# Kernel optimization log

Measured on AMD Instinct MI355X. Metric: run time of the kernel, lower is better.

The kernel has to match this reference:

```python
import jax, jax.numpy as jnp
import numpy as np

NPERSEG = 512
STEP = 256
NSEG = 9            # frames for L=2048 with boundary='zeros', padded=True
NFREQ = 257
NUM_FILTER = 2
PI = 3.1415926      # same constant as source

_win = 0.5 * (1.0 - jnp.cos(2.0 * jnp.pi * jnp.arange(NPERSEG, dtype=jnp.float32) / NPERSEG))  # periodic hann (scipy get_window('hann'))
_win_sum = 256.0    # sum of periodic hann, exact


def _stft(x):
    # x: (B, D, L) real -> scipy.signal.stft(..., nperseg=512, noverlap=256) => (B, D, 257, 9)
    xp = jnp.pad(x, ((0, 0), (0, 0), (STEP, STEP)))  # boundary='zeros'
    idx = jnp.arange(NSEG)[:, None] * STEP + jnp.arange(NPERSEG)[None, :]
    frames = xp[..., idx] * _win                     # (B,D,9,512)
    Z = jnp.fft.rfft(frames, axis=-1) / _win_sum     # scaling='spectrum'
    return jnp.swapaxes(Z, -1, -2)                   # (B,D,257,9)


def _istft(Z):
    # Z: (B,D,257,9) complex -> (B,D,2048) real (scipy.signal.istft inverse)
    xs = jnp.fft.irfft(jnp.swapaxes(Z, -1, -2) * _win_sum, n=NPERSEG, axis=-1) * _win  # (B,D,9,512)
    total = NPERSEG + (NSEG - 1) * STEP  # 2560
    idx = (jnp.arange(NSEG)[:, None] * STEP + jnp.arange(NPERSEG)[None, :]).reshape(-1)
    B, D = Z.shape[0], Z.shape[1]
    x = jnp.zeros((B, D, total), xs.dtype).at[..., idx].add(xs.reshape(B, D, -1))
    norm = jnp.zeros((total,), jnp.float32).at[idx].add(jnp.tile(_win ** 2, NSEG))
    x = x / jnp.where(norm > 1e-10, norm, 1.0)
    return x[..., STEP:total - STEP]  # trim boundary padding -> length 2048


def _cplx(p):
    return p[..., 0] + 1j * p[..., 1]  # torch.view_as_complex


def _filter(x, length, bank):
    # x: (B,S,D) complex; bank: (K,S,D,2). power = x*x/length (complex square, as in source)
    power = x * x / length
    k = jnp.arange(NUM_FILTER, dtype=jnp.float32)
    coef = jnp.cos((2.0 * (k + 1.0) - 1.0) * PI / 2.0 * NUM_FILTER)  # matches source precedence
    return jnp.sum(power[None] * _cplx(bank)[:, None] * coef[:, None, None, None], axis=0)


def _ln(x, g, b):
    m = jnp.mean(x, -1, keepdims=True)
    v = jnp.mean((x - m) ** 2, -1, keepdims=True)
    return (x - m) * jax.lax.rsqrt(v + 1e-5) * g + b


def _addnorm(x, g1, b1, w1, bb1, w2, bb2, g2, b2):
    x = _ln(x, g1, b1)
    h = jax.nn.gelu(x @ w1.T + bb1, approximate=False)  # torch GELU (exact)
    return _ln(h @ w2.T + bb2 + x, g2, b2)


def setup_inputs() -> dict:
    key = jax.random.key(0)
    ks = jax.random.split(key, 12)
    B, D = 8, 768
    d = {}
    d['ecg'] = jax.random.normal(ks[0], (B, 2048, D), jnp.float32)
    d['image'] = jax.random.normal(ks[1], (B, 196, D), jnp.float32)
    d['ecg_filter_bank'] = jax.random.normal(ks[2], (2, 2313, D, 2), jnp.float32)
    d['cxr_filter_bank'] = jax.random.normal(ks[3], (2, 99, D, 2), jnp.float32)
    d['gate_sel'] = jax.random.normal(ks[4], (99, D, 2), jnp.float32)
    d['gate_w'] = jax.random.normal(ks[5], (D, D), jnp.float32) * 0.02
    d['gate_b'] = jnp.zeros((D,), jnp.float32)
    for i, p in enumerate(['e', 'c']):
        d[p + '_ln1_g'] = jnp.ones((D,), jnp.float32)
        d[p + '_ln1_b'] = jnp.zeros((D,), jnp.float32)
        d[p + '_w1'] = jax.random.normal(ks[6 + 2 * i], (D, D), jnp.float32) * 0.02
        d[p + '_b1'] = jnp.zeros((D,), jnp.float32)
        d[p + '_w2'] = jax.random.normal(ks[7 + 2 * i], (D, D), jnp.float32) * 0.02
        d[p + '_b2'] = jnp.zeros((D,), jnp.float32)
        d[p + '_ln2_g'] = jnp.ones((D,), jnp.float32)
        d[p + '_ln2_b'] = jnp.zeros((D,), jnp.float32)
    return d


def reference(ecg, image, ecg_filter_bank, cxr_filter_bank, gate_sel, gate_w, gate_b,
              e_ln1_g, e_ln1_b, e_w1, e_b1, e_w2, e_b2, e_ln2_g, e_ln2_b,
              c_ln1_g, c_ln1_b, c_w1, c_b1, c_w2, c_b2, c_ln2_g, c_ln2_b):
    B, S, D = ecg.shape
    N = image.shape[1]
    # STFT path (source detaches to CPU -> stop_gradient)
    Z = _stft(jnp.swapaxes(jax.lax.stop_gradient(ecg), 1, 2))       # (B,D,257,9)
    _ecg = jnp.transpose(Z, (0, 2, 3, 1)).reshape(B, NFREQ * NSEG, D)
    _img = jnp.fft.rfft(image, axis=1, norm='ortho')                # (B,99,D)
    _ecg = _filter(_ecg, NFREQ * NSEG, ecg_filter_bank)
    _img = _filter(_img, N // 2 + 1, cxr_filter_bank)
    # Cxr2EcgGate: complex selection, avgpool over spatial (real part), 1x1 conv
    gate = jnp.mean((_img * _cplx(gate_sel)).real, axis=1) @ gate_w.T + gate_b  # (B,D)
    ecg_g = _ecg * gate[:, None, :]
    # NOTE: source overwrites gated image with irfft of filtered _image (ecg_gate output unused)
    img_t = jnp.fft.irfft(_img, n=N, axis=1, norm='ortho')          # (B,N,D)
    Zg = jnp.transpose(ecg_g.reshape(B, NFREQ, NSEG, D), (0, 3, 1, 2))
    ecg_t = jnp.swapaxes(_istft(jax.lax.stop_gradient(Zg)), 1, 2)   # (B,2048,D); source detaches before istft
    text = _addnorm(ecg_t + ecg, e_ln1_g, e_ln1_b, e_w1, e_b1, e_w2, e_b2, e_ln2_g, e_ln2_b)
    img = _addnorm(img_t + image, c_ln1_g, c_ln1_b, c_w1, c_b1, c_w2, c_b2, c_ln2_g, c_ln2_b)
    return (text, img)
```

## Files before the change

kernel.cpp:

```cpp
#include <hip/hip_runtime.h>
#include <math.h>

namespace {

constexpr int B_ = 8;
constexpr int S_ = 2048;
constexpr int D_ = 768;
constexpr int N_ = 196;
constexpr int NF_ = 99;
constexpr int NFREQ_ = 257;
constexpr int NSEG_ = 9;
constexpr int NBINS_ = NFREQ_ * NSEG_;
constexpr int NW_ = D_ * D_;
constexpr float TWOPI_ = 6.28318530717958647692f;

using bf16x8 = __attribute__((ext_vector_type(8))) short;
using f32x4  = __attribute__((ext_vector_type(4))) float;

__device__ __forceinline__ int rev9(int x) { return (int)(__brev((unsigned)x) >> 23); }
__device__ __forceinline__ int padz(int i) { return i + (i >> 4); }

__device__ __forceinline__ unsigned short f2bf(float x) {
  unsigned u = __float_as_uint(x);
  u = (u + 0x7FFFu + ((u >> 16) & 1u)) >> 16;
  return (unsigned short)u;
}
__device__ __forceinline__ float bf2f(unsigned short h) {
  return __uint_as_float(((unsigned)h) << 16);
}

__device__ __forceinline__ float gelu_f(float v) {
  const float x = fabsf(v) * 0.70710678118654752440f;
  const float t = 1.0f / fmaf(0.3275911f, x, 1.0f);
  float p = fmaf(fmaf(fmaf(fmaf(1.061405429f, t, -1.453152027f), t, 1.421413741f),
                      t, -0.284496736f), t, 0.254829592f);
  const float e = __expf(-x * x);
  const float er = 1.0f - p * t * e;
  return 0.5f * v * (1.0f + ((v < 0.f) ? -er : er));
}

__device__ __forceinline__ void gload16(const void* g, void* l) {
  __builtin_amdgcn_global_load_lds((const __attribute__((address_space(1))) void*)g,
                                   (__attribute__((address_space(3))) void*)l, 16, 0, 0);
}

__device__ __forceinline__ float2 cmulf(float2 a, float2 b) {
  return make_float2(a.x * b.x - a.y * b.y, a.x * b.y + a.y * b.x);
}
__device__ __forceinline__ float2 cadd(float2 a, float2 b) {
  return make_float2(a.x + b.x, a.y + b.y);
}
__device__ __forceinline__ float2 csub(float2 a, float2 b) {
  return make_float2(a.x - b.x, a.y - b.y);
}

__global__ __launch_bounds__(256) void k_transpose_g(const float* __restrict__ src,
                                                     float* __restrict__ dst,
                                                     int R, int C) {
  __shared__ float tile[32][33];
  const int b = blockIdx.z;
  const int c0 = blockIdx.x * 32;
  const int r0 = blockIdx.y * 32;
  const int tx = threadIdx.x & 31, ty = threadIdx.x >> 5;
  for (int i = ty; i < 32; i += 8)
    tile[i][tx] = src[((size_t)b * R + r0 + i) * C + c0 + tx];
  __syncthreads();
  for (int i = ty; i < 32; i += 8)
    dst[((size_t)b * C + c0 + i) * R + r0 + tx] = tile[tx][i];
}

constexpr int PREP_W = (NW_ + 255) / 256;
constexpr int PREP_WALL = 4 * PREP_W;
constexpr int PREP_FC = (NBINS_ * D_ + 255) / 256;
__global__ __launch_bounds__(256) void k_prep(
    const float* __restrict__ w0, const float* __restrict__ w1,
    const float* __restrict__ w2, const float* __restrict__ w3,
    unsigned short* __restrict__ wbf, const float2* __restrict__ e2,
    float2* __restrict__ FcT, float2* __restrict__ twg) {
  const int bid = blockIdx.x;
  if (bid < PREP_WALL) {
    const int m = bid / PREP_W;
    const int i = (bid - m * PREP_W) * 256 + threadIdx.x;
    if (i >= NW_) return;
    const float* src = (m == 0) ? w0 : (m == 1) ? w1 : (m == 2) ? w2 : w3;
    wbf[(size_t)m * NW_ + i] = f2bf(src[i]);
  } else if (bid < PREP_WALL + PREP_FC) {
    const int o = (bid - PREP_WALL) * 256 + threadIdx.x;
    if (o >= NBINS_ * D_) return;
    const int d = o / NBINS_;
    const int r = o - d * NBINS_;
    const int f = r / NFREQ_;
    const int k = r - f * NFREQ_;
    const int s = k * 9 + f;
    const float2 a = e2[(size_t)s * D_ + d];
    const float2 b = e2[(size_t)(NBINS_ + s) * D_ + d];
    FcT[o] = make_float2(-(a.x + b.x), -(a.y + b.y));
  } else {
    const int i = (bid - PREP_WALL - PREP_FC) * 256 + threadIdx.x;
    if (i >= 511) return;
    const int v = i + 1;
    const int h = 1 << (31 - __clz(v));
    const int j = v - h;
    float sn, cs;
    sincosf((float)j * ((TWOPI_ * 0.5f) / (float)h), &sn, &cs);
    twg[i] = make_float2(cs, sn);
  }
}

__global__ __launch_bounds__(256) void k_img_dft_f(
    const float* __restrict__ image, const float2* __restrict__ bank2,
    const float2* __restrict__ gsel2, float2* __restrict__ imgF,
    float* __restrict__ part) {
  const int fg = blockIdx.x;
  const int f0 = fg * 9;
  const int d = blockIdx.y * 256 + threadIdx.x;
  const int b = blockIdx.z;
  __shared__ float2 tws[9 * N_];
  for (int idx = threadIdx.x; idx < 9 * N_; idx += 256) {
    const int fi = idx / N_;
    const int t = idx - fi * N_;
    const int r = ((f0 + fi) * t) % N_;
    float sn, cs;
    sincosf(TWOPI_ * (float)r / (float)N_, &sn, &cs);
    tws[idx] = make_float2(cs, sn);
  }
  __syncthreads();
  float re[9] = {}, im[9] = {};
  const float* ip = image + (size_t)b * N_ * D_ + d;
  for (int t = 0; t < N_; ++t) {
    const float v = ip[(size_t)t * D_];
#pragma unroll
    for (int fi = 0; fi < 9; ++fi) {
      const float2 w = tws[fi * N_ + t];
      re[fi] = fmaf(v, w.x, re[fi]);
      im[fi] = fmaf(-v, w.y, im[fi]);
    }
  }
  const float sc = 1.0f / (196.0f * 99.0f);
  float gp = 0.f;
#pragma unroll
  for (int fi = 0; fi < 9; ++fi) {
    const int f = f0 + fi;
    const float pr = (re[fi] * re[fi] - im[fi] * im[fi]) * sc;
    const float pi2 = (2.f * re[fi] * im[fi]) * sc;
    const size_t fd = (size_t)f * D_ + d;
    const float2 c0 = bank2[fd];
    const float2 c1 = bank2[(size_t)NF_ * D_ + fd];
    const float fcr = -(c0.x + c1.x), fci = -(c0.y + c1.y);
    const float zr = pr * fcr - pi2 * fci;
    const float zi = pr * fci + pi2 * fcr;
    imgF[(size_t)(b * NF_ + f) * D_ + d] = make_float2(zr, zi);
    const float2 gw = gsel2[fd];
    gp += zr * gw.x - zi * gw.y;
  }
  part[((size_t)b * 11 + fg) * D_ + d] = gp;
}

__global__ __launch_bounds__(256) void k_gate_mm2(const float* __restrict__ part,
                                                  const float* __restrict__ W,
                                                  const float* __restrict__ bias,
                                                  float* __restrict__ gate) {
  __shared__ float row[8][D_];
  __shared__ float red[16][16][8];
  const int tid = threadIdx.x;
  const int d0 = blockIdx.x * 16;
  for (int i = tid; i < 8 * D_; i += 256) {
    const int b = i / D_, e = i - b * D_;
    float s = 0.f;
    for (int p = 0; p < 11; ++p) s += part[((size_t)b * 11 + p) * D_ + e];
    row[b][e] = s * (1.0f / 99.0f);
  }
  __syncthreads();
  const int dl = tid >> 4;
  const int ec = tid & 15;
  const float* w = W + (size_t)(d0 + dl) * D_ + ec * 48;
  float acc[8] = {};
  for (int e = 0; e < 48; e += 4) {
    const float4 wv = *reinterpret_cast<const float4*>(w + e);
    const int eg = ec * 48 + e;
#pragma unroll
    for (int b = 0; b < 8; ++b) {
      acc[b] = fmaf(row[b][eg], wv.x, acc[b]);
      acc[b] = fmaf(row[b][eg + 1], wv.y, acc[b]);
      acc[b] = fmaf(row[b][eg + 2], wv.z, acc[b]);
      acc[b] = fmaf(row[b][eg + 3], wv.w, acc[b]);
    }
  }
#pragma unroll
  for (int b = 0; b < 8; ++b) red[dl][ec][b] = acc[b];
  __syncthreads();
  if (tid < 128) {
    const int dl2 = tid >> 3, b = tid & 7;
    float s = bias[d0 + dl2];
    for (int c = 0; c < 16; ++c) s += red[dl2][c][b];
    gate[b * D_ + d0 + dl2] = s;
  }
}

__global__ __launch_bounds__(256) void k_img_idft(
    const float2* __restrict__ imgF, const float* __restrict__ image,
    float* __restrict__ xi) {
  const int t0 = blockIdx.x * 14;
  const int d = blockIdx.y * 256 + threadIdx.x;
  const int b = blockIdx.z;
  __shared__ float2 tws[14 * NF_];
  for (int idx = threadIdx.x; idx < 14 * NF_; idx += 256) {
    const int ti = idx / NF_;
    const int f = idx - ti * NF_;
    const int r = ((t0 + ti) * f) % N_;
    float sn, cs;
    sincosf(TWOPI_ * (float)r / (float)N_, &sn, &cs);
    tws[idx] = make_float2(cs, sn);
  }
  __syncthreads();
  const float2* zp = imgF + (size_t)b * NF_ * D_ + d;
  const float2 z0 = zp[0];
  const float2 zny = zp[(size_t)(NF_ - 1) * D_];
  float acc[14];
#pragma unroll
  for (int ti = 0; ti < 14; ++ti)
    acc[ti] = z0.x + (((t0 + ti) & 1) ? -zny.x : zny.x);
  for (int f = 1; f < NF_ - 1; ++f) {
    const float2 z = zp[(size_t)f * D_];
#pragma unroll
    for (int ti = 0; ti < 14; ++ti) {
      const float2 w = tws[ti * NF_ + f];
      acc[ti] += 2.f * (z.x * w.x - z.y * w.y);
    }
  }
#pragma unroll
  for (int ti = 0; ti < 14; ++ti) {
    const size_t idx = (size_t)(b * N_ + t0 + ti) * D_ + d;
    xi[idx] = acc[ti] * (1.0f / 14.0f) + image[idx];
  }
}

__global__ __launch_bounds__(256) void k_layernorm_f2b(const float* __restrict__ x,
                                                       const float* __restrict__ g,
                                                       const float* __restrict__ b,
                                                       unsigned short* __restrict__ out) {
  const int row = blockIdx.x;
  const int tid = threadIdx.x;
  const float* xr = x + (size_t)row * D_;
  const float v0 = xr[tid], v1 = xr[tid + 256], v2 = xr[tid + 512];
  float s = v0 + v1 + v2;
  float q = v0 * v0 + v1 * v1 + v2 * v2;
  __shared__ float red[8];
  for (int off = 32; off > 0; off >>= 1) {
    s += __shfl_down(s, off);
    q += __shfl_down(q, off);
  }
  if ((tid & 63) == 0) { red[tid >> 6] = s; red[4 + (tid >> 6)] = q; }
  __syncthreads();
  s = red[0] + red[1] + red[2] + red[3];
  q = red[4] + red[5] + red[6] + red[7];
  const float mean = s * (1.0f / 768.0f);
  const float var = q * (1.0f / 768.0f) - mean * mean;
  const float inv = rsqrtf(var + 1e-5f);
  unsigned short* orow = out + (size_t)row * D_;
  orow[tid]       = f2bf((v0 - mean) * inv * g[tid]       + b[tid]);
  orow[tid + 256] = f2bf((v1 - mean) * inv * g[tid + 256] + b[tid + 256]);
  orow[tid + 512] = f2bf((v2 - mean) * inv * g[tid + 512] + b[tid + 512]);
}

template <int H, int DIR, bool TRIV>
__device__ __forceinline__ void pass8(float2* z, int l,
                                      float2 wa, float2 wb, float2 wc) {
  asm volatile("s_waitcnt lgkmcnt(0)" ::: "memory");
  const float sg = (DIR < 0) ? -1.f : 1.f;
  const int base = (H == 1) ? (l << 3)
                 : (H == 8) ? (((l >> 3) << 6) | (l & 7))
                            : l;
  const float2 x0 = z[padz(base)],         x1 = z[padz(base + H)];
  const float2 x2 = z[padz(base + 2 * H)], x3 = z[padz(base + 3 * H)];
  const float2 x4 = z[padz(base + 4 * H)], x5 = z[padz(base + 5 * H)];
  const float2 x6 = z[padz(base + 6 * H)], x7 = z[padz(base + 7 * H)];
  const float2 WA = make_float2(wa.x, sg * wa.y);
  const float2 WB = make_float2(wb.x, sg * wb.y);
  const float2 WC = make_float2(wc.x, sg * wc.y);
  const float2 WBp = make_float2(-sg * WB.y, sg * WB.x);
  float2 t, u;
  t = TRIV ? x1 : cmulf(x1, WA); const float2 A0 = cadd(x0, t), A1 = csub(x0, t);
  t = TRIV ? x3 : cmulf(x3, WA); const float2 A2 = cadd(x2, t), A3 = csub(x2, t);
  t = TRIV ? x5 : cmulf(x5, WA); const float2 A4 = cadd(x4, t), A5 = csub(x4, t);
  t = TRIV ? x7 : cmulf(x7, WA); const float2 A6 = cadd(x6, t), A7 = csub(x6, t);
  t = TRIV ? A2 : cmulf(A2, WB);
  u = TRIV ? make_float2(-sg * A3.y, sg * A3.x) : cmulf(A3, WBp);
  const float2 B0 = cadd(A0, t), B2 = csub(A0, t);
  const float2 B1 = cadd(A1, u), B3 = csub(A1, u);
  t = TRIV ? A6 : cmulf(A6, WB);
  u = TRIV ? make_float2(-sg * A7.y, sg * A7.x) : cmulf(A7, WBp);
  const float2 B4 = cadd(A4, t), B6 = csub(A4, t);
  const float2 B5 = cadd(A5, u), B7 = csub(A5, u);
  const float r_ = 0.70710678118654752440f;
  const float2 F1 = TRIV ? make_float2(r_, sg * r_)
                         : cmulf(WC, make_float2(r_, sg * r_));
  const float2 F2 = TRIV ? make_float2(0.f, sg)
                         : make_float2(-sg * WC.y, sg * WC.x);
  const float2 F3 = TRIV ? make_float2(-r_, sg * r_)
                         : cmulf(WC, make_float2(-r_, sg * r_));
  t = TRIV ? B4 : cmulf(B4, WC);
  z[padz(base)]         = cadd(B0, t);
  z[padz(base + 4 * H)] = csub(B0, t);
  t = cmulf(B5, F1);
  z[padz(base + H)]     = cadd(B1, t);
  z[padz(base + 5 * H)] = csub(B1, t);
  t = cmulf(B6, F2);
  z[padz(base + 2 * H)] = cadd(B2, t);
  z[padz(base + 6 * H)] = csub(B2, t);
  t = cmulf(B7, F3);
  z[padz(base + 3 * H)] = cadd(B3, t);
  z[padz(base + 7 * H)] = csub(B3, t);
}

template <int FA, int FB>
__device__ __forceinline__ void scatter_buf(float2* z, const float (&s)[8],
                                            float wlo, float whi, int rlo, int rhi) {
  constexpr int iAlo = (FA > 0) ? FA - 1 : 0;
  constexpr int iAhi = (FA < 8) ? FA : 0;
  constexpr int iBlo = (FB > 0) ? FB - 1 : 0;
  constexpr int iBhi = (FB >= 0 && FB < 8) ? FB : 0;
  const float aLo = (FA == 0) ? 0.f : s[iAlo] * wlo;
  const float aHi = (FA == 8) ? 0.f : s[iAhi] * whi;
  const float bLo = (FB <= 0) ? 0.f : s[iBlo] * wlo;
  const float bHi = (FB < 0 || FB == 8) ? 0.f : s[iBhi] * whi;
  z[rlo] = make_float2(aLo, bLo);
  z[rhi] = make_float2(aHi, bHi);
}

template <int FA, int FB>
__device__ __forceinline__ void filt_pack(const float2* z, int k, float g,
                                          float2 cA, float2 cB,
                                          float2& Ck, float2& Cm) {
  const int q = (512 - k) & 511;
  const float2 Zk = z[padz(k)], Zq = z[padz(q)];
  const float sc = 0.5f / 256.f;
  const float ar = (Zk.x + Zq.x) * sc, ai = (Zk.y - Zq.y) * sc;
  float yar, yai, ybr = 0.f, ybi = 0.f;
  {
    const float pr = (ar * ar - ai * ai) * (1.f / 2313.f);
    const float pi = (2.f * ar * ai) * (1.f / 2313.f);
    yar = (pr * cA.x - pi * cA.y) * g;
    yai = (pr * cA.y + pi * cA.x) * g;
  }
  if (FB >= 0) {
    const float br = (Zk.y + Zq.y) * sc, bi = (Zq.x - Zk.x) * sc;
    const float pr = (br * br - bi * bi) * (1.f / 2313.f);
    const float pi = (2.f * br * bi) * (1.f / 2313.f);
    ybr = (pr * cB.x - pi * cB.y) * g;
    ybi = (pr * cB.y + pi * cB.x) * g;
  }
  if (k == 0 || k == 256) {
    Ck = make_float2(yar, ybr);
    Cm = Ck;
  } else {
    Ck = make_float2(yar - ybi, yai + ybr);
    Cm = make_float2(yar + ybi, ybr - yai);
  }
}

template <int FA0, int FB0, int FA1, int FB1, int FA2, int FB2, int FA3, int FB3,
          int NBUF>
__device__ __forceinline__ void ecg_super4(int tid, float g,
                                           const float2* __restrict__ fc,
                                           const float (&s)[8], const float2 (&ptw)[6],
                                           float2 t8, float2* zA, float2* zB,
                                           float2* zC, float2* zD, float* accr) {
  const float c0 = t8.x;
  const float wlo = 0.5f - 0.5f * c0;
  const float whi = 0.5f + 0.5f * c0;
  float2 cA0 = fc[FA0 * 257 + tid];
  float2 cB0 = make_float2(0.f, 0.f), cA1 = cB0, cB1 = cB0;
  float2 cA2 = cB0, cB2 = cB0, cA3 = cB0, cB3 = cB0;
  if (FB0 >= 0) cB0 = fc[FB0 * 257 + tid];
  if (NBUF > 1) { cA1 = fc[FA1 * 257 + tid]; cB1 = fc[FB1 * 257 + tid]; }
  if (NBUF > 2) { cA2 = fc[FA2 * 257 + tid]; cB2 = fc[FB2 * 257 + tid]; }
  if (NBUF > 3) { cA3 = fc[FA3 * 257 + tid]; cB3 = fc[FB3 * 257 + tid]; }
  __syncthreads();
  const int rlo = padz(rev9(tid)), rhi = padz(rev9(tid + 256));
  scatter_buf<FA0, FB0>(zA, s, wlo, whi, rlo, rhi);
  if (NBUF > 1) scatter_buf<FA1, FB1>(zB, s, wlo, whi, rlo, rhi);
  if (NBUF > 2) scatter_buf<FA2, FB2>(zC, s, wlo, whi, rlo, rhi);
  if (NBUF > 3) scatter_buf<FA3, FB3>(zD, s, wlo, whi, rlo, rhi);
  __syncthreads();
  const int wid = tid >> 6, l = tid & 63;
  if (wid < NBUF) {
    float2* zz = (wid == 0) ? zA : (wid == 1) ? zB : (wid == 2) ? zC : zD;
    pass8<1, -1, true>(zz, l, ptw[0], ptw[1], ptw[2]);
    pass8<8, -1, false>(zz, l, ptw[0], ptw[1], ptw[2]);
    pass8<64, -1, false>(zz, l, ptw[3], ptw[4], ptw[5]);
  }
  __syncthreads();
  float2 Ck0, Cm0, Ck1, Cm1, Ck2, Cm2, Ck3, Cm3;
  float2 Cn0, Cn1, Cn2, Cn3, dum;
  filt_pack<FA0, FB0>(zA, tid, g, cA0, cB0, Ck0, Cm0);
  if (NBUF > 1) filt_pack<FA1, FB1>(zB, tid, g, cA1, cB1, Ck1, Cm1);
  if (NBUF > 2) filt_pack<FA2, FB2>(zC, tid, g, cA2, cB2, Ck2, Cm2);
  if (NBUF > 3) filt_pack<FA3, FB3>(zD, tid, g, cA3, cB3, Ck3, Cm3);
  if (tid == 0) {
    float2 nA, nB = make_float2(0.f, 0.f);
    nA = fc[FA0 * 257 + 256];
    if (FB0 >= 0) nB = fc[FB0 * 257 + 256];
    filt_pack<FA0, FB0>(zA, 256, g, nA, nB, Cn0, dum);
    if (NBUF > 1) {
      nA = fc[FA1 * 257 + 256]; nB = fc[FB1 * 257 + 256];
      filt_pack<FA1, FB1>(zB, 256, g, nA, nB, Cn1, dum);
    }
    if (NBUF > 2) {
      nA = fc[FA2 * 257 + 256]; nB = fc[FB2 * 257 + 256];
      filt_pack<FA2, FB2>(zC, 256, g, nA, nB, Cn2, dum);
    }
    if (NBUF > 3) {
      nA = fc[FA3 * 257 + 256]; nB = fc[FB3 * 257 + 256];
      filt_pack<FA3, FB3>(zD, 256, g, nA, nB, Cn3, dum);
    }
  }
  __syncthreads();
  {
    zA[rlo] = Ck0;
    if (NBUF > 1) zB[rlo] = Ck1;
    if (NBUF > 2) zC[rlo] = Ck2;
    if (NBUF > 3) zD[rlo] = Ck3;
    if (tid == 0) {
      zA[padz(1)] = Cn0;
      if (NBUF > 1) zB[padz(1)] = Cn1;
      if (NBUF > 2) zC[padz(1)] = Cn2;
      if (NBUF > 3) zD[padz(1)] = Cn3;
    } else {
      const int rm = padz(rev9(512 - tid));
      zA[rm] = Cm0;
      if (NBUF > 1) zB[rm] = Cm1;
      if (NBUF > 2) zC[rm] = Cm2;
      if (NBUF > 3) zD[rm] = Cm3;
    }
  }
  __syncthreads();
  if (wid < NBUF) {
    float2* zz = (wid == 0) ? zA : (wid == 1) ? zB : (wid == 2) ? zC : zD;
    pass8<1, 1, true>(zz, l, ptw[0], ptw[1], ptw[2]);
    pass8<8, 1, false>(zz, l, ptw[0], ptw[1], ptw[2]);
    pass8<64, 1, false>(zz, l, ptw[3], ptw[4], ptw[5]);
  }
  __syncthreads();
  {
    const float2 vLo = zA[padz(tid)], vHi = zA[padz(tid + 256)];
    accr[FA0] += 0.5f * wlo * vLo.x;
    accr[FA0 + 1] += 0.5f * whi * vHi.x;
    if (FB0 >= 0) {
      accr[FB0] += 0.5f * wlo * vLo.y;
      accr[FB0 + 1] += 0.5f * whi * vHi.y;
    }
    if (NBUF > 1) {
      const float2 uLo = zB[padz(tid)], uHi = zB[padz(tid + 256)];
      accr[FA1] += 0.5f * wlo * uLo.x;
      accr[FA1 + 1] += 0.5f * whi * uHi.x;
      accr[FB1] += 0.5f * wlo * uLo.y;
      accr[FB1 + 1] += 0.5f * whi * uHi.y;
    }
    if (NBUF > 2) {
      const float2 uLo = zC[padz(tid)], uHi = zC[padz(tid + 256)];
      accr[FA2] += 0.5f * wlo * uLo.x;
      accr[FA2 + 1] += 0.5f * whi * uHi.x;
      accr[FB2] += 0.5f * wlo * uLo.y;
      accr[FB2 + 1] += 0.5f * whi * uHi.y;
    }
    if (NBUF > 3) {
      const float2 uLo = zD[padz(tid)], uHi = zD[padz(tid + 256)];
      accr[FA3] += 0.5f * wlo * uLo.x;
      accr[FA3 + 1] += 0.5f * whi * uHi.x;
      accr[FB3] += 0.5f * wlo * uLo.y;
      accr[FB3 + 1] += 0.5f * whi * uHi.y;
    }
  }
}

__global__ __launch_bounds__(256) void k_ecg_fft(
    const float* __restrict__ ecgT, const float2* __restrict__ FcT,
    const float* __restrict__ gate, const float2* __restrict__ twg,
    unsigned short* __restrict__ xtT) {
  const int bd = blockIdx.x;
  const int d = bd % D_;
  const int tid = threadIdx.x;

  __shared__ float2 zA[544], zB[544], zC[544], zD[544];

  float s[8];
  const float* src = ecgT + (size_t)bd * S_;
#pragma unroll
  for (int k = 0; k < 8; ++k) s[k] = src[k * 256 + tid];

  const int l6 = tid & 63;
  float2 ptw[6];
  ptw[0] = twg[7 + (l6 & 7)];
  ptw[1] = twg[15 + (l6 & 7)];
  ptw[2] = twg[31 + (l6 & 7)];
  ptw[3] = twg[63 + l6];
  ptw[4] = twg[127 + l6];
  ptw[5] = twg[255 + l6];
  const float2 t8 = twg[255 + tid];

  const float g = gate[bd];
  const float2* fc = FcT + (size_t)d * NBINS_;
  float accr[10];
#pragma unroll
  for (int i = 0; i < 10; ++i) accr[i] = 0.f;

  ecg_super4<0, 8, 1, 2, 3, 4, 5, 6, 4>(tid, g, fc, s, ptw, t8, zA, zB, zC, zD, accr);
  ecg_super4<7, -1, 0, 0, 0, 0, 0, 0, 1>(tid, g, fc, s, ptw, t8, zA, zB, zC, zD, accr);

  const float c0 = t8.x;
  const float rinv = 1.0f / (0.5f + 0.5f * c0 * c0);
  unsigned short* dst = xtT + (size_t)bd * S_;
#pragma unroll
  for (int i2 = 0; i2 < 8; ++i2)
    dst[i2 * 256 + tid] = f2bf(accr[i2 + 1] * rinv + s[i2]);
}

__global__ __launch_bounds__(256) void k_colstats_bf(const unsigned short* __restrict__ xtT,
                                                     float2* __restrict__ stats) {
  const int b = blockIdx.y;
  const int t0 = blockIdx.x * 128;
  const int tx = threadIdx.x & 63;
  const int ty = threadIdx.x >> 6;
  float s0 = 0.f, q0 = 0.f, s1 = 0.f, q1 = 0.f;
  const unsigned int* base = (const unsigned int*)(xtT + (size_t)b * D_ * S_);
  for (int dd = ty; dd < D_; dd += 4) {
    const unsigned int u = base[(size_t)dd * (S_ / 2) + (t0 >> 1) + tx];
    const float v0 = bf2f((unsigned short)(u & 0xffffu));
    const float v1 = bf2f((unsigned short)(u >> 16));
    s0 += v0; q0 = fmaf(v0, v0, q0);
    s1 += v1; q1 = fmaf(v1, v1, q1);
  }
  __shared__ float sh[4][64][4];
  sh[ty][tx][0] = s0; sh[ty][tx][1] = q0; sh[ty][tx][2] = s1; sh[ty][tx][3] = q1;
  __syncthreads();
  if (ty == 0) {
    s0 = sh[0][tx][0] + sh[1][tx][0] + sh[2][tx][0] + sh[3][tx][0];
    q0 = sh[0][tx][1] + sh[1][tx][1] + sh[2][tx][1] + sh[3][tx][1];
    s1 = sh[0][tx][2] + sh[1][tx][2] + sh[2][tx][2] + sh[3][tx][2];
    q1 = sh[0][tx][3] + sh[1][tx][3] + sh[2][tx][3] + sh[3][tx][3];
    stats[(size_t)b * S_ + t0 + 2 * tx]     = make_float2(s0, q0);
    stats[(size_t)b * S_ + t0 + 2 * tx + 1] = make_float2(s1, q1);
  }
}

__global__ __launch_bounds__(256) void k_transpose_ln(
    const unsigned short* __restrict__ xtT, const float2* __restrict__ stats,
    const float* __restrict__ g, const float* __restrict__ bia,
    unsigned short* __restrict__ xhat) {
  __shared__ float tile[32][33];
  const int b = blockIdx.z;
  const int t0 = blockIdx.x * 32;
  const int d0 = blockIdx.y * 32;
  const int tx = threadIdx.x & 31, ty = threadIdx.x >> 5;
  for (int i = ty; i < 32; i += 8)
    tile[i][tx] = bf2f(xtT[((size_t)b * D_ + d0 + i) * S_ + t0 + tx]);
  __syncthreads();
  const float gv = g[d0 + tx], bv = bia[d0 + tx];
  for (int i = ty; i < 32; i += 8) {
    const float2 st = stats[(size_t)b * S_ + t0 + i];
    const float mean = st.x * (1.0f / 768.0f);
    const float var = st.y * (1.0f / 768.0f) - mean * mean;
    const float inv = rsqrtf(var + 1e-5f);
    xhat[((size_t)b * S_ + t0 + i) * D_ + d0 + tx] =
        f2bf((tile[tx][i] - mean) * inv * gv + bv);
  }
}

__global__ __launch_bounds__(256) void k_layernorm_dual(
    const unsigned short* __restrict__ x1, const float* __restrict__ g1,
    const float* __restrict__ b1, float* __restrict__ o1, int n1,
    const unsigned short* __restrict__ x2, const float* __restrict__ g2,
    const float* __restrict__ b2, float* __restrict__ o2) {
  int row = blockIdx.x;
  const unsigned short* x; const float *g, *b; float* o;
  if (row < n1) { x = x1; g = g1; b = b1; o = o1; }
  else { row -= n1; x = x2; g = g2; b = b2; o = o2; }
  const int tid = threadIdx.x;
  const unsigned short* xr = x + (size_t)row * D_;
  const float v0 = bf2f(xr[tid]), v1 = bf2f(xr[tid + 256]), v2 = bf2f(xr[tid + 512]);
  float s = v0 + v1 + v2;
  float q = v0 * v0 + v1 * v1 + v2 * v2;
  __shared__ float red[8];
  for (int off = 32; off > 0; off >>= 1) {
    s += __shfl_down(s, off);
    q += __shfl_down(q, off);
  }
  if ((tid & 63) == 0) { red[tid >> 6] = s; red[4 + (tid >> 6)] = q; }
  __syncthreads();
  s = red[0] + red[1] + red[2] + red[3];
  q = red[4] + red[5] + red[6] + red[7];
  const float mean = s * (1.0f / 768.0f);
  const float var = q * (1.0f / 768.0f) - mean * mean;
  const float inv = rsqrtf(var + 1e-5f);
  float* orow = o + (size_t)row * D_;
  orow[tid]       = (v0 - mean) * inv * g[tid]       + b[tid];
  orow[tid + 256] = (v1 - mean) * inv * g[tid + 256] + b[tid + 256];
  orow[tid + 512] = (v2 - mean) * inv * g[tid + 512] + b[tid + 512];
}

template <int MODE>
__global__ __launch_bounds__(256) void k_gemm_dual(
    const unsigned short* __restrict__ A1, const unsigned short* __restrict__ W1,
    const float* __restrict__ b1, const unsigned short* __restrict__ r1,
    unsigned short* __restrict__ o1, int M1, int nby1,
    const unsigned short* __restrict__ A2, const unsigned short* __restrict__ W2,
    const float* __restrict__ b2, const unsigned short* __restrict__ r2,
    unsigned short* __restrict__ o2, int M2) {
  __shared__ unsigned short Asm[2][128 * 64];
  __shared__ unsigned short Bsm[2][128 * 64];
  const int tid = threadIdx.x;
  const int lane = tid & 63, wid = tid >> 6;
  const int wr = wid >> 1, wc = wid & 1;
  int bx, by;
  {
    const int nwg = gridDim.x * gridDim.y;
    const int bid = blockIdx.y * gridDim.x + blockIdx.x;
    const int xcd = bid & 7, lin = bid >> 3;
    const int qq = nwg >> 3, rr = nwg & 7;
    const int nbid = (xcd < rr) ? xcd * (qq + 1) + lin
                                : rr * (qq + 1) + (xcd - rr) * qq + lin;
    bx = nbid % gridDim.x;
    by = nbid / gridDim.x;
  }
  const unsigned short* Abf; const unsigned short* Wbf; const float* bias;
  const unsigned short* resid; unsigned short* outb; int M;
  if (by < nby1) { Abf = A1; Wbf = W1; bias = b1; resid = r1; outb = o1; M = M1; }
  else { by -= nby1; Abf = A2; Wbf = W2; bias = b2; resid = r2; outb = o2; M = M2; }
  const int n0 = bx * 128, m0 = by * 128;

  auto STAGE = [&](int buf, int kt) {
    const int k0 = kt * 64;
#pragma unroll
    for (int i = 0; i < 4; ++i) {
      const int c = tid + 256 * i;
      const int row = c >> 3, sl = c & 7;
      const int gsl = sl ^ (row & 7);
      gload16(Abf + (size_t)(m0 + row) * 768 + k0 + gsl * 8, &Asm[buf][c * 8]);
      gload16(Wbf + (size_t)(n0 + row) * 768 + k0 + gsl * 8, &Bsm[buf][c * 8]);
    }
  };

  f32x4 acc[4][4] = {};
  STAGE(0, 0);
  for (int kt = 0; kt < 12; ++kt) {
    const int cur = kt & 1;
    if (kt < 11) {
      STAGE(cur ^ 1, kt + 1);
      asm volatile("s_waitcnt vmcnt(8)" ::: "memory");
    } else {
      asm volatile("s_waitcnt vmcnt(0)" ::: "memory");
    }
    __builtin_amdgcn_sched_barrier(0);
    __builtin_amdgcn_s_barrier();
#pragma unroll
    for (int ks = 0; ks < 2; ++ks) {
      bf16x8 af[4], bfv[4];
#pragma unroll
      for (int mi = 0; mi < 4; ++mi) {
        const int row = wr * 64 + mi * 16 + (lane & 15);
        const int sl = (ks * 4 + (lane >> 4)) ^ (row & 7);
        af[mi] = *(const bf16x8*)((const char*)Asm[cur] + row * 128 + sl * 16);
      }
#pragma unroll
      for (int ni = 0; ni < 4; ++ni) {
        const int row = wc * 64 + ni * 16 + (lane & 15);
        const int sl = (ks * 4 + (lane >> 4)) ^ (row & 7);
        bfv[ni] = *(const bf16x8*)((const char*)Bsm[cur] + row * 128 + sl * 16);
      }
#pragma unroll
      for (int mi = 0; mi < 4; ++mi)
#pragma unroll
        for (int ni = 0; ni < 4; ++ni)
          acc[mi][ni] = __builtin_amdgcn_mfma_f32_16x16x32_bf16(af[mi], bfv[ni],
                                                                acc[mi][ni], 0, 0, 0);
    }
    __builtin_amdgcn_sched_barrier(0);
    __builtin_amdgcn_s_barrier();
  }
#pragma unroll
  for (int mi = 0; mi < 4; ++mi) {
#pragma unroll
    for (int ni = 0; ni < 4; ++ni) {
      const int col = n0 + wc * 64 + ni * 16 + (lane & 15);
#pragma unroll
      for (int e = 0; e < 4; ++e) {
        const int row = m0 + wr * 64 + mi * 16 + (lane >> 4) * 4 + e;
        if (row >= M) continue;
        float v = acc[mi][ni][e] + bias[col];
        if (MODE == 0) {
          v = gelu_f(v);
        } else {
          v += bf2f(resid[(size_t)row * 768 + col]);
        }
        outb[(size_t)row * 768 + col] = f2bf(v);
      }
    }
  }
}

}

extern "C" void kernel_launch(void* const* d_in, const int* in_sizes, int n_in,
                              void* d_out, int out_size, void* d_ws, size_t ws_size,
                              hipStream_t stream) {
  (void)in_sizes; (void)n_in; (void)out_size; (void)ws_size;
  const float* ecg     = (const float*)d_in[0];
  const float* image   = (const float*)d_in[1];
  const float* ebank   = (const float*)d_in[2];
  const float* cbank   = (const float*)d_in[3];
  const float* gsel    = (const float*)d_in[4];
  const float* gw      = (const float*)d_in[5];
  const float* gb      = (const float*)d_in[6];
  const float* e_ln1_g = (const float*)d_in[7];
  const float* e_ln1_b = (const float*)d_in[8];
  const float* e_w1    = (const float*)d_in[9];
  const float* e_b1    = (const float*)d_in[10];
  const float* e_w2    = (const float*)d_in[11];
  const float* e_b2    = (const float*)d_in[12];
  const float* e_ln2_g = (const float*)d_in[13];
  const float* e_ln2_b = (const float*)d_in[14];
  const float* c_ln1_g = (const float*)d_in[15];
  const float* c_ln1_b = (const float*)d_in[16];
  const float* c_w1    = (const float*)d_in[17];
  const float* c_b1    = (const float*)d_in[18];
  const float* c_w2    = (const float*)d_in[19];
  const float* c_b2    = (const float*)d_in[20];
  const float* c_ln2_g = (const float*)d_in[21];
  const float* c_ln2_b = (const float*)d_in[22];

  float* out = (float*)d_out;
  float* ws = (float*)d_ws;

  constexpr size_t TXT = (size_t)8 * 2048 * 768;
  constexpr size_t IMG = (size_t)8 * 196 * 768;

  float* A  = ws;
  float* Bb = A + TXT;
  unsigned short* wbf = (unsigned short*)(Bb + TXT);
  unsigned short* ew1b = wbf;
  unsigned short* ew2b = wbf + NW_;
  unsigned short* cw1b = wbf + 2 * NW_;
  unsigned short* cw2b = wbf + 3 * NW_;
  float* gatev = (float*)(wbf + 4 * (size_t)NW_);
  float2* stats = (float2*)(gatev + 8 * 768);
  float* gpart = (float*)(stats + 8 * 2048);
  float2* twg = (float2*)(gpart + 8 * 11 * 768);

  float2* FcT = (float2*)out;

  unsigned short* xhat = (unsigned short*)A;
  unsigned short* y_tb = (unsigned short*)A + TXT;
  unsigned short* xtT = (unsigned short*)Bb;
  unsigned short* h_t = (unsigned short*)Bb;
  float* Bb2 = Bb + TXT / 2;
  float2* imgF = (float2*)Bb2;
  float* xi = Bb2 + 1216512;
  unsigned short* xh_i = (unsigned short*)(xi + IMG);
  unsigned short* h_i  = xh_i + IMG;
  unsigned short* y_ib = h_i + IMG;

  k_prep<<<PREP_WALL + PREP_FC + 2, 256, 0, stream>>>(
      e_w1, e_w2, c_w1, c_w2, wbf, (const float2*)ebank, FcT, twg);

  k_img_dft_f<<<dim3(11, 3, 8), 256, 0, stream>>>(image, (const float2*)cbank,
                                                  (const float2*)gsel, imgF, gpart);
  k_gate_mm2<<<48, 256, 0, stream>>>(gpart, gw, gb, gatev);
  k_img_idft<<<dim3(14, 3, 8), 256, 0, stream>>>(imgF, image, xi);
  k_layernorm_f2b<<<1568, 256, 0, stream>>>(xi, c_ln1_g, c_ln1_b, xh_i);

  k_transpose_g<<<dim3(24, 64, 8), 256, 0, stream>>>(ecg, A, 2048, 768);
  k_ecg_fft<<<8 * 768, 256, 0, stream>>>(A, FcT, gatev, twg, xtT);
  k_colstats_bf<<<dim3(16, 8), 256, 0, stream>>>(xtT, stats);
  k_transpose_ln<<<dim3(64, 24, 8), 256, 0, stream>>>(xtT, stats, e_ln1_g, e_ln1_b, xhat);

  k_gemm_dual<0><<<dim3(6, 141), 256, 0, stream>>>(
      xhat, ew1b, e_b1, nullptr, h_t, 16384, 128,
      xh_i, cw1b, c_b1, nullptr, h_i, 1568);
  k_gemm_dual<1><<<dim3(6, 141), 256, 0, stream>>>(
      h_t, ew2b, e_b2, xhat, y_tb, 16384, 128,
      h_i, cw2b, c_b2, xh_i, y_ib, 1568);
  k_layernorm_dual<<<16384 + 1568, 256, 0, stream>>>(
      y_tb, e_ln2_g, e_ln2_b, out, 16384,
      y_ib, c_ln2_g, c_ln2_b, out + TXT);
}
```

Before: 413.5 us.

## Pair two channels per block in ECG FFT to pack the odd ninth frame

The ECG STFT/filter/ISTFT kernel now handles two channels (d and d+384) per 512-thread block instead of one channel per 256-thread block. The first eight frames are packed two real frames per complex FFT across eight wavefronts. The leftover ninth frame from both channels is packed into one shared complex FFT, with a separate gate per half via a new gA/gB argument to filt_pack. This removes the round where only one wavefront was busy and halves the block count, at the cost of larger shared memory per block and extra barriers.

```diff
diff --git a/kernel.cpp b/kernel.cpp
--- a/kernel.cpp
+++ b/kernel.cpp
@@ -329,7 +329,7 @@
 }
 
 template <int FA, int FB>
-__device__ __forceinline__ void filt_pack(const float2* z, int k, float g,
+__device__ __forceinline__ void filt_pack(const float2* z, int k, float gA, float gB,
                                           float2 cA, float2 cB,
                                           float2& Ck, float2& Cm) {
   const int q = (512 - k) & 511;
@@ -340,15 +340,15 @@
   {
     const float pr = (ar * ar - ai * ai) * (1.f / 2313.f);
     const float pi = (2.f * ar * ai) * (1.f / 2313.f);
-    yar = (pr * cA.x - pi * cA.y) * g;
-    yai = (pr * cA.y + pi * cA.x) * g;
+    yar = (pr * cA.x - pi * cA.y) * gA;
+    yai = (pr * cA.y + pi * cA.x) * gA;
   }
   if (FB >= 0) {
     const float br = (Zk.y + Zq.y) * sc, bi = (Zq.x - Zk.x) * sc;
     const float pr = (br * br - bi * bi) * (1.f / 2313.f);
     const float pi = (2.f * br * bi) * (1.f / 2313.f);
-    ybr = (pr * cB.x - pi * cB.y) * g;
-    ybi = (pr * cB.y + pi * cB.x) * g;
+    ybr = (pr * cB.x - pi * cB.y) * gB;
+    ybi = (pr * cB.y + pi * cB.x) * gB;
   }
   if (k == 0 || k == 256) {
     Ck = make_float2(yar, ybr);
@@ -359,161 +359,171 @@
   }
 }
 
-template <int FA0, int FB0, int FA1, int FB1, int FA2, int FB2, int FA3, int FB3,
-          int NBUF>
-__device__ __forceinline__ void ecg_super4(int tid, float g,
-                                           const float2* __restrict__ fc,
-                                           const float (&s)[8], const float2 (&ptw)[6],
-                                           float2 t8, float2* zA, float2* zB,
-                                           float2* zC, float2* zD, float* accr) {
-  const float c0 = t8.x;
-  const float wlo = 0.5f - 0.5f * c0;
-  const float whi = 0.5f + 0.5f * c0;
-  float2 cA0 = fc[FA0 * 257 + tid];
-  float2 cB0 = make_float2(0.f, 0.f), cA1 = cB0, cB1 = cB0;
-  float2 cA2 = cB0, cB2 = cB0, cA3 = cB0, cB3 = cB0;
-  if (FB0 >= 0) cB0 = fc[FB0 * 257 + tid];
-  if (NBUF > 1) { cA1 = fc[FA1 * 257 + tid]; cB1 = fc[FB1 * 257 + tid]; }
-  if (NBUF > 2) { cA2 = fc[FA2 * 257 + tid]; cB2 = fc[FB2 * 257 + tid]; }
-  if (NBUF > 3) { cA3 = fc[FA3 * 257 + tid]; cB3 = fc[FB3 * 257 + tid]; }
-  __syncthreads();
-  const int rlo = padz(rev9(tid)), rhi = padz(rev9(tid + 256));
-  scatter_buf<FA0, FB0>(zA, s, wlo, whi, rlo, rhi);
-  if (NBUF > 1) scatter_buf<FA1, FB1>(zB, s, wlo, whi, rlo, rhi);
-  if (NBUF > 2) scatter_buf<FA2, FB2>(zC, s, wlo, whi, rlo, rhi);
-  if (NBUF > 3) scatter_buf<FA3, FB3>(zD, s, wlo, whi, rlo, rhi);
-  __syncthreads();
-  const int wid = tid >> 6, l = tid & 63;
-  if (wid < NBUF) {
-    float2* zz = (wid == 0) ? zA : (wid == 1) ? zB : (wid == 2) ? zC : zD;
-    pass8<1, -1, true>(zz, l, ptw[0], ptw[1], ptw[2]);
-    pass8<8, -1, false>(zz, l, ptw[0], ptw[1], ptw[2]);
-    pass8<64, -1, false>(zz, l, ptw[3], ptw[4], ptw[5]);
-  }
-  __syncthreads();
-  float2 Ck0, Cm0, Ck1, Cm1, Ck2, Cm2, Ck3, Cm3;
-  float2 Cn0, Cn1, Cn2, Cn3, dum;
-  filt_pack<FA0, FB0>(zA, tid, g, cA0, cB0, Ck0, Cm0);
-  if (NBUF > 1) filt_pack<FA1, FB1>(zB, tid, g, cA1, cB1, Ck1, Cm1);
-  if (NBUF > 2) filt_pack<FA2, FB2>(zC, tid, g, cA2, cB2, Ck2, Cm2);
-  if (NBUF > 3) filt_pack<FA3, FB3>(zD, tid, g, cA3, cB3, Ck3, Cm3);
-  if (tid == 0) {
-    float2 nA, nB = make_float2(0.f, 0.f);
-    nA = fc[FA0 * 257 + 256];
-    if (FB0 >= 0) nB = fc[FB0 * 257 + 256];
-    filt_pack<FA0, FB0>(zA, 256, g, nA, nB, Cn0, dum);
-    if (NBUF > 1) {
-      nA = fc[FA1 * 257 + 256]; nB = fc[FB1 * 257 + 256];
-      filt_pack<FA1, FB1>(zB, 256, g, nA, nB, Cn1, dum);
-    }
-    if (NBUF > 2) {
-      nA = fc[FA2 * 257 + 256]; nB = fc[FB2 * 257 + 256];
-      filt_pack<FA2, FB2>(zC, 256, g, nA, nB, Cn2, dum);
-    }
-    if (NBUF > 3) {
-      nA = fc[FA3 * 257 + 256]; nB = fc[FB3 * 257 + 256];
-      filt_pack<FA3, FB3>(zD, 256, g, nA, nB, Cn3, dum);
-    }
-  }
-  __syncthreads();
-  {
-    zA[rlo] = Ck0;
-    if (NBUF > 1) zB[rlo] = Ck1;
-    if (NBUF > 2) zC[rlo] = Ck2;
-    if (NBUF > 3) zD[rlo] = Ck3;
-    if (tid == 0) {
-      zA[padz(1)] = Cn0;
-      if (NBUF > 1) zB[padz(1)] = Cn1;
-      if (NBUF > 2) zC[padz(1)] = Cn2;
-      if (NBUF > 3) zD[padz(1)] = Cn3;
-    } else {
-      const int rm = padz(rev9(512 - tid));
-      zA[rm] = Cm0;
-      if (NBUF > 1) zB[rm] = Cm1;
-      if (NBUF > 2) zC[rm] = Cm2;
-      if (NBUF > 3) zD[rm] = Cm3;
-    }
-  }
-  __syncthreads();
-  if (wid < NBUF) {
-    float2* zz = (wid == 0) ? zA : (wid == 1) ? zB : (wid == 2) ? zC : zD;
-    pass8<1, 1, true>(zz, l, ptw[0], ptw[1], ptw[2]);
-    pass8<8, 1, false>(zz, l, ptw[0], ptw[1], ptw[2]);
-    pass8<64, 1, false>(zz, l, ptw[3], ptw[4], ptw[5]);
-  }
-  __syncthreads();
-  {
-    const float2 vLo = zA[padz(tid)], vHi = zA[padz(tid + 256)];
-    accr[FA0] += 0.5f * wlo * vLo.x;
-    accr[FA0 + 1] += 0.5f * whi * vHi.x;
-    if (FB0 >= 0) {
-      accr[FB0] += 0.5f * wlo * vLo.y;
-      accr[FB0 + 1] += 0.5f * whi * vHi.y;
-    }
-    if (NBUF > 1) {
-      const float2 uLo = zB[padz(tid)], uHi = zB[padz(tid + 256)];
-      accr[FA1] += 0.5f * wlo * uLo.x;
-      accr[FA1 + 1] += 0.5f * whi * uHi.x;
-      accr[FB1] += 0.5f * wlo * uLo.y;
-      accr[FB1 + 1] += 0.5f * whi * uHi.y;
-    }
-    if (NBUF > 2) {
-      const float2 uLo = zC[padz(tid)], uHi = zC[padz(tid + 256)];
-      accr[FA2] += 0.5f * wlo * uLo.x;
-      accr[FA2 + 1] += 0.5f * whi * uHi.x;
-      accr[FB2] += 0.5f * wlo * uLo.y;
-      accr[FB2 + 1] += 0.5f * whi * uHi.y;
-    }
-    if (NBUF > 3) {
-      const float2 uLo = zD[padz(tid)], uHi = zD[padz(tid + 256)];
-      accr[FA3] += 0.5f * wlo * uLo.x;
-      accr[FA3 + 1] += 0.5f * whi * uHi.x;
-      accr[FB3] += 0.5f * wlo * uLo.y;
-      accr[FB3 + 1] += 0.5f * whi * uHi.y;
-    }
-  }
-}
-
-__global__ __launch_bounds__(256) void k_ecg_fft(
+__global__ __launch_bounds__(512) void k_ecg_fft(
     const float* __restrict__ ecgT, const float2* __restrict__ FcT,
     const float* __restrict__ gate, const float2* __restrict__ twg,
     unsigned short* __restrict__ xtT) {
   const int bd = blockIdx.x;
-  const int d = bd % D_;
+  const int b = bd / 384, d0 = bd - (bd / 384) * 384;
   const int tid = threadIdx.x;
-
-  __shared__ float2 zA[544], zB[544], zC[544], zD[544];
+  const int grp = tid >> 8;
+  const int lt = tid & 255;
+  const int wid = tid >> 6;
+  const int l = tid & 63;
+  const int d = d0 + grp * 384;
+  const int myBD = b * 768 + d;
+
+  __shared__ float2 z[8][544];
 
   float s[8];
-  const float* src = ecgT + (size_t)bd * S_;
-#pragma unroll
-  for (int k = 0; k < 8; ++k) s[k] = src[k * 256 + tid];
-
-  const int l6 = tid & 63;
+  const float* src = ecgT + (size_t)myBD * S_;
+#pragma unroll
+  for (int k = 0; k < 8; ++k) s[k] = src[k * 256 + lt];
+
   float2 ptw[6];
-  ptw[0] = twg[7 + (l6 & 7)];
-  ptw[1] = twg[15 + (l6 & 7)];
-  ptw[2] = twg[31 + (l6 & 7)];
-  ptw[3] = twg[63 + l6];
-  ptw[4] = twg[127 + l6];
-  ptw[5] = twg[255 + l6];
-  const float2 t8 = twg[255 + tid];
-
-  const float g = gate[bd];
+  ptw[0] = twg[7 + (l & 7)];
+  ptw[1] = twg[15 + (l & 7)];
+  ptw[2] = twg[31 + (l & 7)];
+  ptw[3] = twg[63 + l];
+  ptw[4] = twg[127 + l];
+  ptw[5] = twg[255 + l];
+  const float2 t8 = twg[255 + lt];
+  const float c0 = t8.x;
+  const float wlo = 0.5f - 0.5f * c0;
+  const float whi = 0.5f + 0.5f * c0;
+  const int rlo = padz(rev9(lt)), rhi = padz(rev9(lt + 256));
+
+  const float gX = gate[b * 768 + d0];
+  const float gY = gate[b * 768 + d0 + 384];
+  const float gOwn = grp ? gY : gX;
   const float2* fc = FcT + (size_t)d * NBINS_;
+
   float accr[10];
 #pragma unroll
   for (int i = 0; i < 10; ++i) accr[i] = 0.f;
 
-  ecg_super4<0, 8, 1, 2, 3, 4, 5, 6, 4>(tid, g, fc, s, ptw, t8, zA, zB, zC, zD, accr);
-  ecg_super4<7, -1, 0, 0, 0, 0, 0, 0, 1>(tid, g, fc, s, ptw, t8, zA, zB, zC, zD, accr);
-
-  const float c0 = t8.x;
+  const float2 cA0 = fc[0 * 257 + lt], cB0 = fc[8 * 257 + lt];
+  const float2 cA1 = fc[1 * 257 + lt], cB1 = fc[2 * 257 + lt];
+  const float2 cA2 = fc[3 * 257 + lt], cB2 = fc[4 * 257 + lt];
+  const float2 cA3 = fc[5 * 257 + lt], cB3 = fc[6 * 257 + lt];
+  float2* zg = z[grp * 4];
+  scatter_buf<0, 8>(z[grp * 4 + 0], s, wlo, whi, rlo, rhi);
+  scatter_buf<1, 2>(z[grp * 4 + 1], s, wlo, whi, rlo, rhi);
+  scatter_buf<3, 4>(z[grp * 4 + 2], s, wlo, whi, rlo, rhi);
+  scatter_buf<5, 6>(z[grp * 4 + 3], s, wlo, whi, rlo, rhi);
+  __syncthreads();
+  {
+    float2* zz = z[wid];
+    pass8<1, -1, true>(zz, l, ptw[0], ptw[1], ptw[2]);
+    pass8<8, -1, false>(zz, l, ptw[0], ptw[1], ptw[2]);
+    pass8<64, -1, false>(zz, l, ptw[3], ptw[4], ptw[5]);
+  }
+  __syncthreads();
+  float2 Ck0, Cm0, Ck1, Cm1, Ck2, Cm2, Ck3, Cm3;
+  float2 Cn0, Cn1, Cn2, Cn3, dum;
+  filt_pack<0, 8>(z[grp * 4 + 0], lt, gOwn, gOwn, cA0, cB0, Ck0, Cm0);
+  filt_pack<1, 2>(z[grp * 4 + 1], lt, gOwn, gOwn, cA1, cB1, Ck1, Cm1);
+  filt_pack<3, 4>(z[grp * 4 + 2], lt, gOwn, gOwn, cA2, cB2, Ck2, Cm2);
+  filt_pack<5, 6>(z[grp * 4 + 3], lt, gOwn, gOwn, cA3, cB3, Ck3, Cm3);
+  if (lt == 0) {
+    float2 nA, nB;
+    nA = fc[0 * 257 + 256]; nB = fc[8 * 257 + 256];
+    filt_pack<0, 8>(z[grp * 4 + 0], 256, gOwn, gOwn, nA, nB, Cn0, dum);
+    nA = fc[1 * 257 + 256]; nB = fc[2 * 257 + 256];
+    filt_pack<1, 2>(z[grp * 4 + 1], 256, gOwn, gOwn, nA, nB, Cn1, dum);
+    nA = fc[3 * 257 + 256]; nB = fc[4 * 257 + 256];
+    filt_pack<3, 4>(z[grp * 4 + 2], 256, gOwn, gOwn, nA, nB, Cn2, dum);
+    nA = fc[5 * 257 + 256]; nB = fc[6 * 257 + 256];
+    filt_pack<5, 6>(z[grp * 4 + 3], 256, gOwn, gOwn, nA, nB, Cn3, dum);
+  }
+  __syncthreads();
+  {
+    zg[0 * 544 + rlo] = Ck0; zg[1 * 544 + rlo] = Ck1;
+    zg[2 * 544 + rlo] = Ck2; zg[3 * 544 + rlo] = Ck3;
+    if (lt == 0) {
+      zg[0 * 544 + padz(1)] = Cn0; zg[1 * 544 + padz(1)] = Cn1;
+      zg[2 * 544 + padz(1)] = Cn2; zg[3 * 544 + padz(1)] = Cn3;
+    } else {
+      const int rm = padz(rev9(512 - lt));
+      zg[0 * 544 + rm] = Cm0; zg[1 * 544 + rm] = Cm1;
+      zg[2 * 544 + rm] = Cm2; zg[3 * 544 + rm] = Cm3;
+    }
+  }
+  __syncthreads();
+  {
+    float2* zz = z[wid];
+    pass8<1, 1, true>(zz, l, ptw[0], ptw[1], ptw[2]);
+    pass8<8, 1, false>(zz, l, ptw[0], ptw[1], ptw[2]);
+    pass8<64, 1, false>(zz, l, ptw[3], ptw[4], ptw[5]);
+  }
+  __syncthreads();
+  {
+    float2 vLo, vHi;
+    vLo = zg[0 * 544 + padz(lt)]; vHi = zg[0 * 544 + padz(lt + 256)];
+    accr[0] += 0.5f * wlo * vLo.x; accr[1] += 0.5f * whi * vHi.x;
+    accr[8] += 0.5f * wlo * vLo.y; accr[9] += 0.5f * whi * vHi.y;
+    vLo = zg[1 * 544 + padz(lt)]; vHi = zg[1 * 544 + padz(lt + 256)];
+    accr[1] += 0.5f * wlo * vLo.x; accr[2] += 0.5f * whi * vHi.x;
+    accr[2] += 0.5f * wlo * vLo.y; accr[3] += 0.5f * whi * vHi.y;
+    vLo = zg[2 * 544 + padz(lt)]; vHi = zg[2 * 544 + padz(lt + 256)];
+    accr[3] += 0.5f * wlo * vLo.x; accr[4] += 0.5f * whi * vHi.x;
+    accr[4] += 0.5f * wlo * vLo.y; accr[5] += 0.5f * whi * vHi.y;
+    vLo = zg[3 * 544 + padz(lt)]; vHi = zg[3 * 544 + padz(lt + 256)];
+    accr[5] += 0.5f * wlo * vLo.x; accr[6] += 0.5f * whi * vHi.x;
+    accr[6] += 0.5f * wlo * vLo.y; accr[7] += 0.5f * whi * vHi.y;
+  }
+  __syncthreads();
+
+  {
+    float* z0f = (float*)z[0];
+    z0f[2 * rlo + grp] = s[6] * wlo;
+    z0f[2 * rhi + grp] = s[7] * whi;
+  }
+  __syncthreads();
+  if (wid == 0) {
+    pass8<1, -1, true>(z[0], l, ptw[0], ptw[1], ptw[2]);
+    pass8<8, -1, false>(z[0], l, ptw[0], ptw[1], ptw[2]);
+    pass8<64, -1, false>(z[0], l, ptw[3], ptw[4], ptw[5]);
+  }
+  __syncthreads();
+  float2 CkC, CmC, CnC;
+  if (grp == 0) {
+    const float2* fcY = FcT + (size_t)(d0 + 384) * NBINS_;
+    const float2 cA = fc[7 * 257 + lt];
+    const float2 cB = fcY[7 * 257 + lt];
+    filt_pack<7, 7>(z[0], lt, gX, gY, cA, cB, CkC, CmC);
+    if (lt == 0) {
+      const float2 nA = fc[7 * 257 + 256];
+      const float2 nB = fcY[7 * 257 + 256];
+      filt_pack<7, 7>(z[0], 256, gX, gY, nA, nB, CnC, dum);
+    }
+  }
+  __syncthreads();
+  if (grp == 0) {
+    z[0][rlo] = CkC;
+    if (lt == 0) z[0][padz(1)] = CnC;
+    else z[0][padz(rev9(512 - lt))] = CmC;
+  }
+  __syncthreads();
+  if (wid == 0) {
+    pass8<1, 1, true>(z[0], l, ptw[0], ptw[1], ptw[2]);
+    pass8<8, 1, false>(z[0], l, ptw[0], ptw[1], ptw[2]);
+    pass8<64, 1, false>(z[0], l, ptw[3], ptw[4], ptw[5]);
+  }
+  __syncthreads();
+  {
+    const float2 vLo = z[0][padz(lt)], vHi = z[0][padz(lt + 256)];
+    const float xlo = grp ? vLo.y : vLo.x;
+    const float xhi = grp ? vHi.y : vHi.x;
+    accr[7] += 0.5f * wlo * xlo;
+    accr[8] += 0.5f * whi * xhi;
+  }
+
   const float rinv = 1.0f / (0.5f + 0.5f * c0 * c0);
-  unsigned short* dst = xtT + (size_t)bd * S_;
+  unsigned short* dst = xtT + (size_t)myBD * S_;
 #pragma unroll
   for (int i2 = 0; i2 < 8; ++i2)
-    dst[i2 * 256 + tid] = f2bf(accr[i2 + 1] * rinv + s[i2]);
+    dst[i2 * 256 + lt] = f2bf(accr[i2 + 1] * rinv + s[i2]);
 }
 
 __global__ __launch_bounds__(256) void k_colstats_bf(const unsigned short* __restrict__ xtT,
@@ -770,7 +780,7 @@
   k_layernorm_f2b<<<1568, 256, 0, stream>>>(xi, c_ln1_g, c_ln1_b, xh_i);
 
   k_transpose_g<<<dim3(24, 64, 8), 256, 0, stream>>>(ecg, A, 2048, 768);
-  k_ecg_fft<<<8 * 768, 256, 0, stream>>>(A, FcT, gatev, twg, xtT);
+  k_ecg_fft<<<3072, 512, 0, stream>>>(A, FcT, gatev, twg, xtT);
   k_colstats_bf<<<dim3(16, 8), 256, 0, stream>>>(xtT, stats);
   k_transpose_ln<<<dim3(64, 24, 8), 256, 0, stream>>>(xtT, stats, e_ln1_g, e_ln1_b, xhat);
 
```

Measured after the change: 450.5 us (median of 3 runs). 8.9% more time.
